# Optimization experiments

Measured on AMD Instinct MI355X. Metric: run time of the kernel, lower is better.

The kernel has to match this reference:

```python
import jax, jax.numpy as jnp
import numpy as np

H = 1024   # hidden_size
B, S, L = 8, 4096, 64


def setup_inputs() -> dict:
    key = jax.random.key(0)
    k1, k2, k3 = jax.random.split(key, 3)
    hidden = jax.random.normal(k1, (L, B, H), dtype=jnp.float32)
    encoder_states = jax.random.normal(k2, (B, S, 2 * H), dtype=jnp.float32)
    # nn.Linear(2H, H): weight [H, 2H], bias [H]
    W = jax.random.normal(k3, (H, 2 * H), dtype=jnp.float32) * (1.0 / np.sqrt(2 * H))
    b = jnp.zeros((H,), dtype=jnp.float32)
    return {"hidden": hidden, "encoder_states": encoder_states, "W": W, "b": b}


def reference(hidden, encoder_states, W, b):
    # fc projection: [B,S,2H] @ [2H,H] -> [B,S,H]
    reduced = jnp.einsum('bsk,hk->bsh', encoder_states, W) + b
    # scores: bmm(reduced [B,S,H], hidden.permute(1,2,0) [B,H,L]) -> [B,S,L]
    scores = jnp.einsum('bsh,lbh->bsl', reduced, hidden)
    # softmax over encoder positions (dim=1)
    weights = jax.nn.softmax(scores, axis=1)
    # context: bmm(weights^T [B,L,S], reduced [B,S,H]) -> [B,L,H]
    context = jnp.einsum('bsl,bsh->blh', weights, reduced)
    return context, weights
```

## Files before the change

### kernel.cpp

```cpp
#include <hip/hip_runtime.h>


#define H_ 1024
#define B_ 8
#define S_ 4096
#define L_ 64
#define K2H 2048

typedef _Float16 f16x8 __attribute__((ext_vector_type(8)));
typedef _Float16 f16x4 __attribute__((ext_vector_type(4)));
typedef float f32x4 __attribute__((ext_vector_type(4)));


__global__ __launch_bounds__(256) void kcast_kernel(const float* __restrict__ src,
                                                    _Float16* __restrict__ hi,
                                                    _Float16* __restrict__ lo) {
    __shared__ float T[16][516];
    const int t = threadIdx.x;
    const int slab = blockIdx.x, ksec = blockIdx.y;
    const float* sp = src + (size_t)slab * 16 * K2H + ksec * 512;
#pragma unroll
    for (int r = 0; r < 8; r++) {
        int lin = r * 1024 + t * 4;
        int row = lin >> 9, col = lin & 511;
        float4 v = *(const float4*)(sp + (size_t)row * K2H + col);
        T[row][col] = v.x; T[row][col + 1] = v.y; T[row][col + 2] = v.z; T[row][col + 3] = v.w;
    }
    __syncthreads();
    const size_t obase = ((size_t)slab * 64 + ksec * 16) * 512;
#pragma unroll
    for (int r = 0; r < 4; r++) {
        int c = r * 256 + t;
        int kt = c >> 6, lam = c & 63;
        int m = lam & 15, kb = kt * 32 + (lam >> 4) * 8;
        f16x8 h, l;
#pragma unroll
        for (int e = 0; e < 8; e++) {
            float x = T[m][kb + e];
            _Float16 hh = (_Float16)x;
            h[e] = hh;
            l[e] = (_Float16)(x - (float)hh);
        }
        *(f16x8*)(hi + obase + (size_t)c * 8) = h;
        if (lo) *(f16x8*)(lo + obase + (size_t)c * 8) = l;
    }
}

__global__ __launch_bounds__(256, 4) void kcs_kernel(const float* __restrict__ enc,
                                                     _Float16* __restrict__ enc16,
                                                     const _Float16* __restrict__ vh,
                                                     const _Float16* __restrict__ vl,
                                                     float* __restrict__ scores) {
    __shared__ _Float16 TT[2][16][520];
    const int t = threadIdx.x;
    const int slab = blockIdx.x;
    const int b = slab >> 8;
    const int w = t >> 6, lane = t & 63;
    const int ml = lane & 15, q = lane >> 4;
    f32x4 acc[4] = {};

    const float* sp0 = enc + (size_t)slab * (16 * K2H);
    float4 rbuf[8];
#pragma unroll
    for (int r = 0; r < 8; r++) {
        int lin = r * 1024 + t * 4;
        rbuf[r] = *(const float4*)(sp0 + (size_t)(lin >> 9) * K2H + (lin & 511));
    }

    for (int ksec = 0; ksec < 4; ksec++) {
#pragma unroll
        for (int r = 0; r < 8; r++) {
            int lin = r * 1024 + t * 4;
            int row = lin >> 9, col = lin & 511;
            float4 v = rbuf[r];
            f16x4 h4, l4;
            h4[0] = (_Float16)v.x; h4[1] = (_Float16)v.y;
            h4[2] = (_Float16)v.z; h4[3] = (_Float16)v.w;
            l4[0] = (_Float16)(v.x - (float)h4[0]);
            l4[1] = (_Float16)(v.y - (float)h4[1]);
            l4[2] = (_Float16)(v.z - (float)h4[2]);
            l4[3] = (_Float16)(v.w - (float)h4[3]);
            *(f16x4*)&TT[0][row][col] = h4;
            *(f16x4*)&TT[1][row][col] = l4;
            *(f16x4*)(enc16 + ((size_t)(slab * 16 + row)) * K2H + ksec * 512 + col) = h4;
        }
        __syncthreads();
        if (ksec < 3) {
            const float* sp = sp0 + (ksec + 1) * 512;
#pragma unroll
            for (int r = 0; r < 8; r++) {
                int lin = r * 1024 + t * 4;
                rbuf[r] = *(const float4*)(sp + (size_t)(lin >> 9) * K2H + (lin & 511));
            }
        }
#pragma unroll
        for (int r = 0; r < 4; r++) {
            const int ktl = r * 4 + w;
            const int kb = ktl * 32 + q * 8;
            f16x8 h = *(const f16x8*)&TT[0][ml][kb];
            f16x8 l = *(const f16x8*)&TT[1][ml][kb];
            const int ktg = ksec * 16 + ktl;
            const size_t vbase = (((size_t)(b * 4) * 64) + ktg) * 512 + (size_t)lane * 8;
#pragma unroll
            for (int lt = 0; lt < 4; lt++) {
                f16x8 bH = *(const f16x8*)(vh + vbase + (size_t)lt * 32768);
                f16x8 bL = *(const f16x8*)(vl + vbase + (size_t)lt * 32768);
                acc[lt] = __builtin_amdgcn_mfma_f32_16x16x32_f16(h, bH, acc[lt], 0, 0, 0);
                acc[lt] = __builtin_amdgcn_mfma_f32_16x16x32_f16(l, bH, acc[lt], 0, 0, 0);
                acc[lt] = __builtin_amdgcn_mfma_f32_16x16x32_f16(h, bL, acc[lt], 0, 0, 0);
            }
        }
        __syncthreads();
    }
    float (*P)[16][66] = reinterpret_cast<float (*)[16][66]>(&TT[0][0][0]);
#pragma unroll
    for (int lt = 0; lt < 4; lt++)
#pragma unroll
        for (int r = 0; r < 4; r++)
            P[w][q * 4 + r][lt * 16 + ml] = acc[lt][r];
    __syncthreads();
    const int s0 = (slab & 255) * 16;
#pragma unroll
    for (int u = 0; u < 4; u++) {
        const int idx = u * 256 + t;
        const int srow = idx >> 6, l = idx & 63;
        float v = P[0][srow][l] + P[1][srow][l] + P[2][srow][l] + P[3][srow][l];
        scores[(size_t)b * (S_ * L_) + (size_t)(s0 + srow) * L_ + l] = v;
    }
}

__global__ __launch_bounds__(256) void kv2_kernel(const float* __restrict__ hidden,
                                                  const float* __restrict__ W,
                                                  _Float16* __restrict__ vh,
                                                  _Float16* __restrict__ vl) {
    __shared__ float Ah[64][17];
    __shared__ float Wt[16][64];
    const int b = blockIdx.x;
    const int k0 = blockIdx.y * 64;
    const int t = threadIdx.x;
    const int lt = t & 15, kt = t >> 4;
    float acc[4][4];
#pragma unroll
    for (int i = 0; i < 4; i++)
#pragma unroll
        for (int j = 0; j < 4; j++) acc[i][j] = 0.f;

    const int ar = t >> 2, ac4 = (t & 3) * 4;
    const int wrow = t >> 4, wc4 = (t & 15) * 4;

    for (int h0 = 0; h0 < H_; h0 += 16) {
        float4 av = *(const float4*)(hidden + (size_t)ar * (B_ * H_) + b * H_ + h0 + ac4);
        Ah[ar][ac4 + 0] = av.x; Ah[ar][ac4 + 1] = av.y; Ah[ar][ac4 + 2] = av.z; Ah[ar][ac4 + 3] = av.w;
        *(float4*)&Wt[wrow][wc4] = *(const float4*)(W + (size_t)(h0 + wrow) * K2H + k0 + wc4);
        __syncthreads();
#pragma unroll
        for (int hh = 0; hh < 16; hh++) {
            float a0 = Ah[lt * 4 + 0][hh], a1 = Ah[lt * 4 + 1][hh];
            float a2 = Ah[lt * 4 + 2][hh], a3 = Ah[lt * 4 + 3][hh];
            float4 wv = *(const float4*)&Wt[hh][kt * 4];
            acc[0][0] += a0 * wv.x; acc[0][1] += a0 * wv.y; acc[0][2] += a0 * wv.z; acc[0][3] += a0 * wv.w;
            acc[1][0] += a1 * wv.x; acc[1][1] += a1 * wv.y; acc[1][2] += a1 * wv.z; acc[1][3] += a1 * wv.w;
            acc[2][0] += a2 * wv.x; acc[2][1] += a2 * wv.y; acc[2][2] += a2 * wv.z; acc[2][3] += a2 * wv.w;
            acc[3][0] += a3 * wv.x; acc[3][1] += a3 * wv.y; acc[3][2] += a3 * wv.z; acc[3][3] += a3 * wv.w;
        }
        __syncthreads();
    }
#pragma unroll
    for (int i = 0; i < 4; i++) {
        const int l = lt * 4 + i;
        const int ltile = l >> 4, lam = l & 15;
#pragma unroll
        for (int j = 0; j < 4; j++) {
            const int k = k0 + kt * 4 + j;
            const size_t idx = (((size_t)(b * 4 + ltile) * 64) + (k >> 5)) * 512
                             + (size_t)((((k >> 3) & 3) * 16 + lam) * 8 + (k & 7));
            float v = acc[i][j];
            _Float16 hh = (_Float16)v;
            vh[idx] = hh;
            vl[idx] = (_Float16)(v - (float)hh);
        }
    }
}

__global__ __launch_bounds__(256) void kU_kernel(const _Float16* __restrict__ wa,
                                                 const _Float16* __restrict__ enc16,
                                                 float* __restrict__ Upart) {
    __shared__ _Float16 T[32][66];
    const int t = threadIdx.x;
    const int b = blockIdx.x, nc = blockIdx.y, ks = blockIdx.z;
    const int w = t >> 6, lane = t & 63;
    const int ml = lane & 15, q = lane >> 4;
    const int wm = w >> 1, wn = w & 1;
    f32x4 acc[2][2] = {};
    const int srow = t >> 3, scol = (t & 7) * 8;

    for (int it = 0; it < 32; ++it) {
        const int s0 = ks * 1024 + it * 32;
        *(f16x8*)&T[srow][scol] =
            *(const f16x8*)(enc16 + ((size_t)(b * S_ + s0 + srow)) * K2H + nc * 64 + scol);
        __syncthreads();
        f16x8 bf[2];
#pragma unroll
        for (int j = 0; j < 2; j++) {
            const int cb = (wn * 2 + j) * 16 + ml;
#pragma unroll
            for (int e = 0; e < 8; e++) bf[j][e] = T[q * 8 + e][cb];
        }
        const int stile = ks * 32 + it;
#pragma unroll
        for (int i = 0; i < 2; i++) {
            f16x8 a = *(const f16x8*)(wa + (((size_t)(b * 4 + wm * 2 + i)) * 128 + stile) * 512
                                       + (size_t)lane * 8);
#pragma unroll
            for (int j = 0; j < 2; j++)
                acc[i][j] = __builtin_amdgcn_mfma_f32_16x16x32_f16(a, bf[j], acc[i][j], 0, 0, 0);
        }
        __syncthreads();
    }
#pragma unroll
    for (int i = 0; i < 2; i++)
#pragma unroll
        for (int j = 0; j < 2; j++)
#pragma unroll
            for (int r = 0; r < 4; r++) {
                const int l = wm * 32 + i * 16 + q * 4 + r;
                const int ch = nc * 64 + (wn * 2 + j) * 16 + ml;
                Upart[(((size_t)(ks * 8 + b)) * 64 + l) * K2H + ch] = acc[i][j][r];
            }
}

__global__ __launch_bounds__(256) void kC_kernel(const float* __restrict__ Upart,
                                                 const _Float16* __restrict__ w16h,
                                                 const _Float16* __restrict__ w16l,
                                                 const float* __restrict__ bias,
                                                 float* __restrict__ ctx) {
    __shared__ _Float16 AsH[64][40], AsL[64][40];
    const int t = threadIdx.x;
    const int hc = blockIdx.x, b = blockIdx.y;
    const int w = t >> 6, lane = t & 63;
    const int ml = lane & 15, q = lane >> 4;
    const int wm = w >> 1, wn = w & 1;
    f32x4 acc[2][2] = {};
    const int r0 = t >> 2, c8 = (t & 3) * 8;

    for (int k0 = 0; k0 < K2H; k0 += 32) {
        float xv[8];
#pragma unroll
        for (int e = 0; e < 8; e++) xv[e] = 0.f;
        const size_t ub = ((size_t)b * 64 + r0) * K2H + k0 + c8;
#pragma unroll
        for (int p = 0; p < 4; p++) {
            const float* up = Upart + (size_t)p * (8 * 64 * K2H) + ub;
            float4 u0 = *(const float4*)up, u1 = *(const float4*)(up + 4);
            xv[0] += u0.x; xv[1] += u0.y; xv[2] += u0.z; xv[3] += u0.w;
            xv[4] += u1.x; xv[5] += u1.y; xv[6] += u1.z; xv[7] += u1.w;
        }
        f16x8 hh, ll;
#pragma unroll
        for (int e = 0; e < 8; e++) {
            _Float16 hv = (_Float16)xv[e];
            hh[e] = hv;
            ll[e] = (_Float16)(xv[e] - (float)hv);
        }
        *(f16x8*)&AsH[r0][c8] = hh;
        *(f16x8*)&AsL[r0][c8] = ll;
        __syncthreads();
        const int kt = k0 >> 5;
        f16x8 bH[2], bL[2];
#pragma unroll
        for (int j = 0; j < 2; j++) {
            const size_t wb = (((size_t)(hc * 4 + wn * 2 + j)) * 64 + kt) * 512 + (size_t)lane * 8;
            bH[j] = *(const f16x8*)(w16h + wb);
            bL[j] = *(const f16x8*)(w16l + wb);
        }
#pragma unroll
        for (int i = 0; i < 2; i++) {
            f16x8 aH = *(const f16x8*)&AsH[wm * 32 + i * 16 + ml][q * 8];
            f16x8 aL = *(const f16x8*)&AsL[wm * 32 + i * 16 + ml][q * 8];
#pragma unroll
            for (int j = 0; j < 2; j++) {
                acc[i][j] = __builtin_amdgcn_mfma_f32_16x16x32_f16(aH, bH[j], acc[i][j], 0, 0, 0);
                acc[i][j] = __builtin_amdgcn_mfma_f32_16x16x32_f16(aL, bH[j], acc[i][j], 0, 0, 0);
                acc[i][j] = __builtin_amdgcn_mfma_f32_16x16x32_f16(aH, bL[j], acc[i][j], 0, 0, 0);
            }
        }
        __syncthreads();
    }
#pragma unroll
    for (int i = 0; i < 2; i++)
#pragma unroll
        for (int j = 0; j < 2; j++) {
            const int h = hc * 64 + wn * 32 + j * 16 + ml;
            const float bv = bias[h];
#pragma unroll
            for (int r = 0; r < 4; r++) {
                const int l = wm * 32 + i * 16 + q * 4 + r;
                ctx[(((size_t)(b * 64 + l)) << 10) + h] = acc[i][j][r] + bv;
            }
        }
}


__global__ __launch_bounds__(256) void ksb_kernel(const float* __restrict__ hidden,
                                                  const float* __restrict__ bias,
                                                  float* __restrict__ sb) {
    const int b = blockIdx.x, t = threadIdx.x;
    const int l = t & 63, j = t >> 6;
    const float* hp = hidden + (size_t)l * (B_ * H_) + b * H_ + j * 256;
    const float* bp = bias + j * 256;
    float s = 0.f;
    for (int i = 0; i < 64; i++) {
        float4 h4 = *(const float4*)(hp + i * 4);
        float4 b4 = *(const float4*)(bp + i * 4);
        s += h4.x * b4.x + h4.y * b4.y + h4.z * b4.z + h4.w * b4.w;
    }
    __shared__ float red[256];
    red[t] = s; __syncthreads();
    if (t < 128) red[t] += red[t + 128];
    __syncthreads();
    if (t < 64) sb[b * 64 + t] = red[t] + red[t + 64];
}

__global__ __launch_bounds__(256) void kv_kernel(const float* __restrict__ hidden,
                                                 const float* __restrict__ W,
                                                 float* __restrict__ V) {
    __shared__ float Ah[64][17];
    __shared__ float Wt[16][64];
    const int b = blockIdx.x;
    const int k0 = blockIdx.y * 64;
    const int t = threadIdx.x;
    const int lt = t & 15, kt = t >> 4;
    float acc[4][4];
#pragma unroll
    for (int i = 0; i < 4; i++)
#pragma unroll
        for (int j = 0; j < 4; j++) acc[i][j] = 0.f;

    const int ar = t >> 2, ac4 = (t & 3) * 4;
    const int wrow = t >> 4, wc4 = (t & 15) * 4;

    for (int h0 = 0; h0 < H_; h0 += 16) {
        float4 av = *(const float4*)(hidden + (size_t)ar * (B_ * H_) + b * H_ + h0 + ac4);
        Ah[ar][ac4 + 0] = av.x; Ah[ar][ac4 + 1] = av.y; Ah[ar][ac4 + 2] = av.z; Ah[ar][ac4 + 3] = av.w;
        *(float4*)&Wt[wrow][wc4] = *(const float4*)(W + (size_t)(h0 + wrow) * K2H + k0 + wc4);
        __syncthreads();
#pragma unroll
        for (int hh = 0; hh < 16; hh++) {
            float a0 = Ah[lt * 4 + 0][hh], a1 = Ah[lt * 4 + 1][hh];
            float a2 = Ah[lt * 4 + 2][hh], a3 = Ah[lt * 4 + 3][hh];
            float4 wv = *(const float4*)&Wt[hh][kt * 4];
            acc[0][0] += a0 * wv.x; acc[0][1] += a0 * wv.y; acc[0][2] += a0 * wv.z; acc[0][3] += a0 * wv.w;
            acc[1][0] += a1 * wv.x; acc[1][1] += a1 * wv.y; acc[1][2] += a1 * wv.z; acc[1][3] += a1 * wv.w;
            acc[2][0] += a2 * wv.x; acc[2][1] += a2 * wv.y; acc[2][2] += a2 * wv.z; acc[2][3] += a2 * wv.w;
            acc[3][0] += a3 * wv.x; acc[3][1] += a3 * wv.y; acc[3][2] += a3 * wv.z; acc[3][3] += a3 * wv.w;
        }
        __syncthreads();
    }
#pragma unroll
    for (int i = 0; i < 4; i++) {
        float4 o; o.x = acc[i][0]; o.y = acc[i][1]; o.z = acc[i][2]; o.w = acc[i][3];
        *(float4*)(V + (size_t)b * (L_ * K2H) + (lt * 4 + i) * K2H + k0 + kt * 4) = o;
    }
}

__global__ __launch_bounds__(256) void k1_kernel(const float* __restrict__ enc,
                                                 const float* __restrict__ W,
                                                 const float* __restrict__ bias,
                                                 _Float16* __restrict__ reduced) {
    __shared__ _Float16 As[128][40];
    __shared__ _Float16 Bs[128][40];
    const int t = threadIdx.x;
    const int n0 = blockIdx.x * 128;
    const int m0 = blockIdx.y * 128;
    const int w = t >> 6, lane = t & 63;
    const int wr = w >> 1, wc = w & 1;
    const int ml = lane & 15, q = lane >> 4;

    f32x4 acc[4][4];
#pragma unroll
    for (int i = 0; i < 4; i++)
#pragma unroll
        for (int j = 0; j < 4; j++) acc[i][j] = (f32x4){0.f, 0.f, 0.f, 0.f};

    const int r0 = t >> 2;
    const int c8 = (t & 3) * 8;

    for (int k0 = 0; k0 < K2H; k0 += 32) {
#pragma unroll
        for (int j = 0; j < 2; ++j) {
            const int row = r0 + 64 * j;
            const float* pa = enc + (size_t)(m0 + row) * K2H + k0 + c8;
            float4 a0 = *(const float4*)pa, a1 = *(const float4*)(pa + 4);
            f16x8 ha;
            ha[0] = (_Float16)a0.x; ha[1] = (_Float16)a0.y; ha[2] = (_Float16)a0.z; ha[3] = (_Float16)a0.w;
            ha[4] = (_Float16)a1.x; ha[5] = (_Float16)a1.y; ha[6] = (_Float16)a1.z; ha[7] = (_Float16)a1.w;
            *(f16x8*)&As[row][c8] = ha;
            const float* pb = W + (size_t)(n0 + row) * K2H + k0 + c8;
            float4 b0 = *(const float4*)pb, b1 = *(const float4*)(pb + 4);
            f16x8 hb;
            hb[0] = (_Float16)b0.x; hb[1] = (_Float16)b0.y; hb[2] = (_Float16)b0.z; hb[3] = (_Float16)b0.w;
            hb[4] = (_Float16)b1.x; hb[5] = (_Float16)b1.y; hb[6] = (_Float16)b1.z; hb[7] = (_Float16)b1.w;
            *(f16x8*)&Bs[row][c8] = hb;
        }
        __syncthreads();
        f16x8 af[4], bf[4];
#pragma unroll
        for (int i = 0; i < 4; i++) af[i] = *(const f16x8*)&As[wr * 64 + i * 16 + ml][q * 8];
#pragma unroll
        for (int j = 0; j < 4; j++) bf[j] = *(const f16x8*)&Bs[wc * 64 + j * 16 + ml][q * 8];
#pragma unroll
        for (int i = 0; i < 4; i++)
#pragma unroll
            for (int j = 0; j < 4; j++)
                acc[i][j] = __builtin_amdgcn_mfma_f32_16x16x32_f16(af[i], bf[j], acc[i][j], 0, 0, 0);
        __syncthreads();
    }
#pragma unroll
    for (int j = 0; j < 4; j++) {
        const int h = n0 + wc * 64 + j * 16 + ml;
        const float bv = bias[h];
#pragma unroll
        for (int i = 0; i < 4; i++) {
            const int srow = m0 + wr * 64 + i * 16 + q * 4;
#pragma unroll
            for (int r = 0; r < 4; r++)
                reduced[(size_t)(srow + r) * H_ + h] = (_Float16)(acc[i][j][r] + bv);
        }
    }
}

__global__ __launch_bounds__(256) void ks_kernel(const float* __restrict__ enc,
                                                 const float* __restrict__ V,
                                                 const float* __restrict__ sb,
                                                 float* __restrict__ scores) {
    __shared__ _Float16 AsH[64][40], AsL[64][40];
    __shared__ _Float16 BsH[64][40], BsL[64][40];
    const int t = threadIdx.x;
    const int s0 = blockIdx.x * 64;
    const int b = blockIdx.y;
    const int w = t >> 6, lane = t & 63;
    const int ml = lane & 15, q = lane >> 4;

    f32x4 acc[4];
#pragma unroll
    for (int j = 0; j < 4; j++) acc[j] = (f32x4){0.f, 0.f, 0.f, 0.f};

    const int r0 = t >> 2, c8 = (t & 3) * 8;

    for (int k0 = 0; k0 < K2H; k0 += 32) {
        {
            const float* pa = enc + (size_t)(b * S_ + s0 + r0) * K2H + k0 + c8;
            float4 a0 = *(const float4*)pa, a1 = *(const float4*)(pa + 4);
            float xv[8] = {a0.x, a0.y, a0.z, a0.w, a1.x, a1.y, a1.z, a1.w};
            f16x8 hh, ll;
#pragma unroll
            for (int e = 0; e < 8; e++) {
                _Float16 hi = (_Float16)xv[e];
                hh[e] = hi;
                ll[e] = (_Float16)(xv[e] - (float)hi);
            }
            *(f16x8*)&AsH[r0][c8] = hh;
            *(f16x8*)&AsL[r0][c8] = ll;
        }
        {
            const float* pb = V + (size_t)b * (L_ * K2H) + (size_t)r0 * K2H + k0 + c8;
            float4 b0 = *(const float4*)pb, b1 = *(const float4*)(pb + 4);
            float xv[8] = {b0.x, b0.y, b0.z, b0.w, b1.x, b1.y, b1.z, b1.w};
            f16x8 hh, ll;
#pragma unroll
            for (int e = 0; e < 8; e++) {
                _Float16 hi = (_Float16)xv[e];
                hh[e] = hi;
                ll[e] = (_Float16)(xv[e] - (float)hi);
            }
            *(f16x8*)&BsH[r0][c8] = hh;
            *(f16x8*)&BsL[r0][c8] = ll;
        }
        __syncthreads();
        f16x8 aH = *(const f16x8*)&AsH[w * 16 + ml][q * 8];
        f16x8 aL = *(const f16x8*)&AsL[w * 16 + ml][q * 8];
#pragma unroll
        for (int j = 0; j < 4; j++) {
            f16x8 bH = *(const f16x8*)&BsH[j * 16 + ml][q * 8];
            f16x8 bL = *(const f16x8*)&BsL[j * 16 + ml][q * 8];
            acc[j] = __builtin_amdgcn_mfma_f32_16x16x32_f16(aH, bH, acc[j], 0, 0, 0);
            acc[j] = __builtin_amdgcn_mfma_f32_16x16x32_f16(aL, bH, acc[j], 0, 0, 0);
            acc[j] = __builtin_amdgcn_mfma_f32_16x16x32_f16(aH, bL, acc[j], 0, 0, 0);
        }
        __syncthreads();
    }
#pragma unroll
    for (int j = 0; j < 4; j++) {
        const int l = j * 16 + ml;
        const float sbv = sb[b * 64 + l];
        const int srow = s0 + w * 16 + q * 4;
#pragma unroll
        for (int r = 0; r < 4; r++)
            scores[(size_t)b * (S_ * L_) + (size_t)(srow + r) * L_ + l] = acc[j][r] + sbv;
    }
}

__global__ __launch_bounds__(256) void k4_kernel(const float* __restrict__ wbuf,
                                                 const _Float16* __restrict__ reduced,
                                                 float* __restrict__ ctx) {
    __shared__ float Ws[64][64];
    __shared__ _Float16 Rs[64][256];
    const int t = threadIdx.x;
    const int b = blockIdx.x, ht = blockIdx.y, sc = blockIdx.z;
    const int h = ht * 256 + t;
    float acc[64];
#pragma unroll
    for (int l = 0; l < 64; l++) acc[l] = 0.f;

    for (int cc = 0; cc < 4; ++cc) {
        const int sbase = sc * 256 + cc * 64;
#pragma unroll
        for (int j = 0; j < 4; j++) {
            int c = t + 256 * j;
            int row = c >> 4, c4 = (c & 15) * 4;
            *(float4*)&Ws[row][c4] =
                *(const float4*)(wbuf + (size_t)b * (S_ * L_) + (size_t)(sbase + row) * L_ + c4);
        }
#pragma unroll
        for (int j = 0; j < 8; j++) {
            int c = t + 256 * j;
            int row = c >> 5, ch = (c & 31) * 8;
            *(uint4*)&Rs[row][ch] =
                *(const uint4*)(reduced + (size_t)(b * S_ + sbase + row) * H_ + ht * 256 + ch);
        }
        __syncthreads();
        for (int ss = 0; ss < 64; ++ss) {
            float r = (float)Rs[ss][t];
            const float4* wr = (const float4*)&Ws[ss][0];
#pragma unroll
            for (int u = 0; u < 16; u++) {
                float4 wv = wr[u];
                acc[u * 4 + 0] += wv.x * r;
                acc[u * 4 + 1] += wv.y * r;
                acc[u * 4 + 2] += wv.z * r;
                acc[u * 4 + 3] += wv.w * r;
            }
        }
        __syncthreads();
    }
#pragma unroll
    for (int l = 0; l < 64; l++)
        atomicAdd(ctx + (size_t)((b * 64 + l) << 10) + h, acc[l]);
}


__global__ __launch_bounds__(256) void k3a_kernel(const float* __restrict__ scores,
                                                  float* __restrict__ partM,
                                                  float* __restrict__ partD) {
    const int b = blockIdx.x, chunk = blockIdx.y;
    const int t = threadIdx.x;
    const int l = t & 63, si = t >> 6;
    const float* p = scores + (size_t)b * (S_ * L_) + (size_t)(chunk * 256 + si * 64) * L_ + l;
    float m = -__builtin_inff(), d = 0.f;
    for (int i = 0; i < 64; i++) {
        float x = p[i * 64];
        if (x > m) { d = d * __expf(m - x) + 1.f; m = x; }
        else d += __expf(x - m);
    }
    __shared__ float sm[256], sd[256];
    sm[t] = m; sd[t] = d; __syncthreads();
    if (t < 128) {
        float m2 = sm[t + 128], d2 = sd[t + 128];
        if (m2 > sm[t]) { sd[t] = sd[t] * __expf(sm[t] - m2) + d2; sm[t] = m2; }
        else sd[t] += d2 * __expf(m2 - sm[t]);
    }
    __syncthreads();
    if (t < 64) {
        float m1 = sm[t], d1 = sd[t], m2 = sm[t + 64], d2 = sd[t + 64];
        if (m2 > m1) { d1 = d1 * __expf(m1 - m2) + d2; m1 = m2; }
        else d1 += d2 * __expf(m2 - m1);
        partM[(b * 16 + chunk) * 64 + t] = m1;
        partD[(b * 16 + chunk) * 64 + t] = d1;
    }
}

__global__ __launch_bounds__(512) void k3b_kernel(const float* __restrict__ partM,
                                                  const float* __restrict__ partD,
                                                  float* __restrict__ fm,
                                                  float* __restrict__ fdinv) {
    const int t = threadIdx.x;
    const int b = t >> 6, l = t & 63;
    float m = -__builtin_inff(), d = 0.f;
    for (int c = 0; c < 16; c++) {
        float pm = partM[(b * 16 + c) * 64 + l];
        float pd = partD[(b * 16 + c) * 64 + l];
        if (pm > m) { d = d * __expf(m - pm) + pd; m = pm; }
        else d += pd * __expf(pm - m);
    }
    fm[t] = m;
    fdinv[t] = 1.0f / d;
}

__global__ __launch_bounds__(256) void k3c_kernel(float* __restrict__ wbuf,
                                                  const float* __restrict__ fm,
                                                  const float* __restrict__ fdinv,
                                                  _Float16* __restrict__ watile) {
    const int t = threadIdx.x;
    const int l = t & 63;
    const int g = blockIdx.x * 4 + (t >> 6);
    const int b = g >> 9;
    const int s0 = (g & 511) * 8;
    const float m = fm[b * 64 + l];
    const float inv = fdinv[b * 64 + l];
    float* wp = wbuf + (size_t)b * (S_ * L_) + (size_t)s0 * L_ + l;
    float y[8];
#pragma unroll
    for (int i = 0; i < 8; i++) y[i] = __expf(wp[i * L_] - m) * inv;
#pragma unroll
    for (int i = 0; i < 8; i++) wp[i * L_] = y[i];
    if (watile) {
        f16x8 o;
#pragma unroll
        for (int i = 0; i < 8; i++) o[i] = (_Float16)y[i];
        const size_t woff = (((size_t)(b * 4 + (l >> 4)) * 128) + (s0 >> 5)) * 512
                          + (size_t)((((s0 >> 3) & 3) * 16 + (l & 15)) * 8);
        *(f16x8*)(watile + woff) = o;
    }
}

extern "C" void kernel_launch(void* const* d_in, const int* in_sizes, int n_in,
                              void* d_out, int out_size, void* d_ws, size_t ws_size,
                              hipStream_t stream) {
    const float* hidden = (const float*)d_in[0];
    const float* enc    = (const float*)d_in[1];
    const float* W      = (const float*)d_in[2];
    const float* bias   = (const float*)d_in[3];

    float* ctx  = (float*)d_out;
    float* wbuf = (float*)d_out + (B_ * L_ * H_);

    char* ws = (char*)d_ws;
    const size_t NEED_FAST = 209784832;

    if (ws_size >= NEED_FAST) {
        _Float16* enc16 = (_Float16*)ws;
        float*    Upart = (float*)(ws + 134217728);
        _Float16* w16h  = (_Float16*)(ws + 150994944);
        _Float16* w16l  = (_Float16*)(ws + 155189248);
        _Float16* vh    = (_Float16*)(ws + 159383552);
        _Float16* vl    = (_Float16*)(ws + 161480704);
        _Float16* watile = vh;
        float* partM = (float*)(ws + 163577856);
        float* partD = partM + 8 * 16 * 64;
        float* fm    = partD + 8 * 16 * 64;
        float* fdinv = fm + 512;

        kv2_kernel<<<dim3(8, 32), 256, 0, stream>>>(hidden, W, vh, vl);
        kcast_kernel<<<dim3(64, 4), 256, 0, stream>>>(W, w16h, w16l);
        kcs_kernel<<<2048, 256, 0, stream>>>(enc, enc16, vh, vl, wbuf);
        k3a_kernel<<<dim3(8, 16), 256, 0, stream>>>(wbuf, partM, partD);
        k3b_kernel<<<1, 512, 0, stream>>>(partM, partD, fm, fdinv);
        k3c_kernel<<<1024, 256, 0, stream>>>(wbuf, fm, fdinv, watile);
        kU_kernel<<<dim3(8, 32, 4), 256, 0, stream>>>(watile, enc16, Upart);
        kC_kernel<<<dim3(16, 8), 256, 0, stream>>>(Upart, w16h, w16l, bias, ctx);
    } else {
        _Float16* reduced = (_Float16*)ws;
        float* V     = (float*)(ws + 67108864);
        float* partM = (float*)(ws + 71303168);
        float* partD = partM + 8 * 16 * 64;
        float* fm    = partD + 8 * 16 * 64;
        float* fdinv = fm + 512;
        float* sb    = fdinv + 512;

        hipMemsetAsync(ctx, 0, (size_t)B_ * L_ * H_ * sizeof(float), stream);
        ksb_kernel<<<8, 256, 0, stream>>>(hidden, bias, sb);
        kv_kernel<<<dim3(8, 32), 256, 0, stream>>>(hidden, W, V);
        k1_kernel<<<dim3(8, 256), 256, 0, stream>>>(enc, W, bias, reduced);
        ks_kernel<<<dim3(64, 8), 256, 0, stream>>>(enc, V, sb, wbuf);
        k3a_kernel<<<dim3(8, 16), 256, 0, stream>>>(wbuf, partM, partD);
        k3b_kernel<<<1, 512, 0, stream>>>(partM, partD, fm, fdinv);
        k3c_kernel<<<1024, 256, 0, stream>>>(wbuf, fm, fdinv, (_Float16*)nullptr);
        k4_kernel<<<dim3(8, 4, 16), 256, 0, stream>>>(wbuf, reduced, ctx);
    }
}
```

Baseline: 711.2 us.

## Store fp16 encoder in MFMA-tiled layout and split context GEMM over K

The scores kernel now writes the fp16 copy of the encoder states already transposed into MFMA B-operand tiles. This lets the U kernel load fragments straight from global memory with no shared-memory staging or barriers. Separately, the final context kernel is split four ways along K and accumulates into a zeroed output with atomicAdd, which adds a memset and atomic traffic in exchange for more blocks. The transposing write reads shared memory column-wise, which may cause bank conflicts and extra work in the scores kernel.

```diff
diff --git a/kernel.cpp b/kernel.cpp
--- a/kernel.cpp
+++ b/kernel.cpp
@@ -47,7 +47,7 @@
 }
 
 __global__ __launch_bounds__(256, 4) void kcs_kernel(const float* __restrict__ enc,
-                                                     _Float16* __restrict__ enc16,
+                                                     _Float16* __restrict__ encB,
                                                      const _Float16* __restrict__ vh,
                                                      const _Float16* __restrict__ vl,
                                                      float* __restrict__ scores) {
@@ -66,6 +66,8 @@
         int lin = r * 1024 + t * 4;
         rbuf[r] = *(const float4*)(sp0 + (size_t)(lin >> 9) * K2H + (lin & 511));
     }
+    const int qb = (slab & 1) * 2;
+    const int st = (slab & 255) >> 1;
 
     for (int ksec = 0; ksec < 4; ksec++) {
 #pragma unroll
@@ -82,7 +84,6 @@
             l4[3] = (_Float16)(v.w - (float)h4[3]);
             *(f16x4*)&TT[0][row][col] = h4;
             *(f16x4*)&TT[1][row][col] = l4;
-            *(f16x4*)(enc16 + ((size_t)(slab * 16 + row)) * K2H + ksec * 512 + col) = h4;
         }
         __syncthreads();
         if (ksec < 3) {
@@ -92,6 +93,20 @@
                 int lin = r * 1024 + t * 4;
                 rbuf[r] = *(const float4*)(sp + (size_t)(lin >> 9) * K2H + (lin & 511));
             }
+        }
+#pragma unroll
+        for (int p = 0; p < 4; p++) {
+            const int pid = p * 256 + t;
+            const int ctl = pid >> 5;
+            const int w5 = pid & 31;
+            const int oct = w5 >> 4, c = w5 & 15;
+            f16x8 v;
+#pragma unroll
+            for (int e = 0; e < 8; e++) v[e] = TT[0][oct * 8 + e][ctl * 16 + c];
+            const int ctg = ksec * 32 + ctl;
+            const size_t off = (((size_t)(b * 128 + ctg)) * 128 + st) * 512
+                             + (size_t)((qb + oct) * 16 + c) * 8;
+            *(f16x8*)(encB + off) = v;
         }
 #pragma unroll
         for (int r = 0; r < 4; r++) {
@@ -183,30 +198,24 @@
 }
 
 __global__ __launch_bounds__(256) void kU_kernel(const _Float16* __restrict__ wa,
-                                                 const _Float16* __restrict__ enc16,
+                                                 const _Float16* __restrict__ encB,
                                                  float* __restrict__ Upart) {
-    __shared__ _Float16 T[32][66];
     const int t = threadIdx.x;
     const int b = blockIdx.x, nc = blockIdx.y, ks = blockIdx.z;
     const int w = t >> 6, lane = t & 63;
     const int ml = lane & 15, q = lane >> 4;
     const int wm = w >> 1, wn = w & 1;
     f32x4 acc[2][2] = {};
-    const int srow = t >> 3, scol = (t & 7) * 8;
 
     for (int it = 0; it < 32; ++it) {
-        const int s0 = ks * 1024 + it * 32;
-        *(f16x8*)&T[srow][scol] =
-            *(const f16x8*)(enc16 + ((size_t)(b * S_ + s0 + srow)) * K2H + nc * 64 + scol);
-        __syncthreads();
+        const int stile = ks * 32 + it;
         f16x8 bf[2];
 #pragma unroll
         for (int j = 0; j < 2; j++) {
-            const int cb = (wn * 2 + j) * 16 + ml;
-#pragma unroll
-            for (int e = 0; e < 8; e++) bf[j][e] = T[q * 8 + e][cb];
-        }
-        const int stile = ks * 32 + it;
+            const int ct = nc * 4 + wn * 2 + j;
+            bf[j] = *(const f16x8*)(encB + (((size_t)(b * 128 + ct)) * 128 + stile) * 512
+                                     + (size_t)lane * 8);
+        }
 #pragma unroll
         for (int i = 0; i < 2; i++) {
             f16x8 a = *(const f16x8*)(wa + (((size_t)(b * 4 + wm * 2 + i)) * 128 + stile) * 512
@@ -215,7 +224,6 @@
             for (int j = 0; j < 2; j++)
                 acc[i][j] = __builtin_amdgcn_mfma_f32_16x16x32_f16(a, bf[j], acc[i][j], 0, 0, 0);
         }
-        __syncthreads();
     }
 #pragma unroll
     for (int i = 0; i < 2; i++)
@@ -236,14 +244,14 @@
                                                  float* __restrict__ ctx) {
     __shared__ _Float16 AsH[64][40], AsL[64][40];
     const int t = threadIdx.x;
-    const int hc = blockIdx.x, b = blockIdx.y;
+    const int hc = blockIdx.x, b = blockIdx.y, kq = blockIdx.z;
     const int w = t >> 6, lane = t & 63;
     const int ml = lane & 15, q = lane >> 4;
     const int wm = w >> 1, wn = w & 1;
     f32x4 acc[2][2] = {};
     const int r0 = t >> 2, c8 = (t & 3) * 8;
 
-    for (int k0 = 0; k0 < K2H; k0 += 32) {
+    for (int k0 = kq * 512; k0 < kq * 512 + 512; k0 += 32) {
         float xv[8];
 #pragma unroll
         for (int e = 0; e < 8; e++) xv[e] = 0.f;
@@ -291,11 +299,11 @@
 #pragma unroll
         for (int j = 0; j < 2; j++) {
             const int h = hc * 64 + wn * 32 + j * 16 + ml;
-            const float bv = bias[h];
+            const float bv = (kq == 0) ? bias[h] : 0.f;
 #pragma unroll
             for (int r = 0; r < 4; r++) {
                 const int l = wm * 32 + i * 16 + q * 4 + r;
-                ctx[(((size_t)(b * 64 + l)) << 10) + h] = acc[i][j][r] + bv;
+                atomicAdd(ctx + (((size_t)(b * 64 + l)) << 10) + h, acc[i][j][r] + bv);
             }
         }
 }
@@ -638,7 +646,7 @@
     const size_t NEED_FAST = 209784832;
 
     if (ws_size >= NEED_FAST) {
-        _Float16* enc16 = (_Float16*)ws;
+        _Float16* encB  = (_Float16*)ws;
         float*    Upart = (float*)(ws + 134217728);
         _Float16* w16h  = (_Float16*)(ws + 150994944);
         _Float16* w16l  = (_Float16*)(ws + 155189248);
@@ -650,14 +658,15 @@
         float* fm    = partD + 8 * 16 * 64;
         float* fdinv = fm + 512;
 
+        hipMemsetAsync(ctx, 0, (size_t)B_ * L_ * H_ * sizeof(float), stream);
         kv2_kernel<<<dim3(8, 32), 256, 0, stream>>>(hidden, W, vh, vl);
         kcast_kernel<<<dim3(64, 4), 256, 0, stream>>>(W, w16h, w16l);
-        kcs_kernel<<<2048, 256, 0, stream>>>(enc, enc16, vh, vl, wbuf);
+        kcs_kernel<<<2048, 256, 0, stream>>>(enc, encB, vh, vl, wbuf);
         k3a_kernel<<<dim3(8, 16), 256, 0, stream>>>(wbuf, partM, partD);
         k3b_kernel<<<1, 512, 0, stream>>>(partM, partD, fm, fdinv);
         k3c_kernel<<<1024, 256, 0, stream>>>(wbuf, fm, fdinv, watile);
-        kU_kernel<<<dim3(8, 32, 4), 256, 0, stream>>>(watile, enc16, Upart);
-        kC_kernel<<<dim3(16, 8), 256, 0, stream>>>(Upart, w16h, w16l, bias, ctx);
+        kU_kernel<<<dim3(8, 32, 4), 256, 0, stream>>>(watile, encB, Upart);
+        kC_kernel<<<dim3(16, 8, 4), 256, 0, stream>>>(Upart, w16h, w16l, bias, ctx);
     } else {
         _Float16* reduced = (_Float16*)ws;
         float* V     = (float*)(ws + 67108864);
```

Result: faster. 639.0 us (-10.2%).
